# Kernel tuning notes

Hardware: AMD Instinct MI355X
Metric: run time of the kernel (lower is better)

## Reference

```python
import jax, jax.numpy as jnp
import numpy as np

B, N, D, H, WIN = 8, 4096, 768, 8, 8
HD = D // H
FG = N // 2 + 1
FL = WIN // 2 + 1


def _gelu(x):
    return jax.nn.gelu(x, approximate=False)


def _cgelu(z):
    # magnitude-based complex GELU: z * gelu(|z|) / (|z| + 1e-6)
    mag = jnp.abs(z)
    return z * (_gelu(mag) / (mag + 1e-6))


def setup_inputs():
    key = jax.random.key(0)
    ks = jax.random.split(key, 8)

    def w(k, shape):
        return jax.random.normal(k, shape, dtype=jnp.float32) * 0.02

    return {
        "x": jax.random.normal(ks[0], (B, N, D), dtype=jnp.float32),
        "ln_w": jnp.ones((D,), jnp.float32),
        "ln_b": jnp.zeros((D,), jnp.float32),
        "bf_g": jnp.ones((H, FG, 1), jnp.float32),
        "bb_g": jnp.full((H, FG, 1), -0.1, jnp.float32),
        "bf_l": jnp.ones((H, FL, 1), jnp.float32),
        "bb_l": jnp.full((H, FL, 1), -0.1, jnp.float32),
        "w1g": w(ks[1], (D, D)),
        "b1g": jnp.zeros((D,), jnp.float32),
        "w2g": w(ks[2], (D, H * FG * 2)),
        "b2g": jnp.zeros((H * FG * 2,), jnp.float32),
        "w1l": w(ks[3], (D, D)),
        "b1l": jnp.zeros((D,), jnp.float32),
        "w2l": w(ks[4], (D, H * FL * 2)),
        "b2l": jnp.zeros((H * FL * 2,), jnp.float32),
        "wf1": w(ks[5], (D, D // 2)),
        "bf1": jnp.zeros((D // 2,), jnp.float32),
        "wf2": w(ks[6], (D // 2, H)),
        "bf2": jnp.zeros((H,), jnp.float32),
    }


def reference(x, ln_w, ln_b, bf_g, bb_g, bf_l, bb_l, w1g, b1g, w2g, b2g,
              w1l, b1l, w2l, b2l, wf1, bf1, wf2, bf2):
    # pre-norm (LayerNorm, eps=1e-5)
    mu = jnp.mean(x, axis=-1, keepdims=True)
    var = jnp.mean((x - mu) ** 2, axis=-1, keepdims=True)
    xn = (x - mu) / jnp.sqrt(var + 1e-5) * ln_w + ln_b
    xh = xn.reshape(B, N, H, HD).transpose(0, 2, 1, 3)  # (B,H,N,HD)
    ctx = xn.mean(axis=1)  # (B,D)

    # ---- global branch: Hann-windowed rFFT over full sequence ----
    ag = (_gelu(ctx @ w1g + b1g) @ w2g + b2g).reshape(B, H, FG, 2)
    hann_g = jnp.hanning(N).astype(x.dtype)[None, None, :, None]
    Ff = jnp.fft.rfft(xh * hann_g, axis=2, norm="ortho")  # (B,H,FG,HD) complex
    eff_f = bf_g[None] * (1.0 + ag[..., 0:1])
    eff_b = bb_g[None] + ag[..., 1:2]
    x_global = jnp.fft.irfft(_cgelu(Ff * eff_f + eff_b), n=N, axis=2, norm="ortho")

    al = (_gelu(ctx @ w1l + b1l) @ w2l + b2l).reshape(B, H, FL, 2)
    nw = N // WIN
    hann_l = jnp.hanning(WIN).astype(x.dtype)[None, None, None, :, None]
    xw = xh.reshape(B, H, nw, WIN, HD) * hann_l
    Fl_fft = jnp.fft.rfft(xw, axis=3, norm="ortho")  # (B,H,nw,FL,HD)
    eff_fl = bf_l[None, :, None] * (1.0 + al[:, :, None, :, 0:1])
    eff_bl = bb_l[None, :, None] + al[:, :, None, :, 1:2]
    x_local = jnp.fft.irfft(_cgelu(Fl_fft * eff_fl + eff_bl), n=WIN, axis=3,
                            norm="ortho").reshape(B, H, N, HD)

    # ---- fusion gate ----
    alpha = jax.nn.sigmoid(_gelu(ctx @ wf1 + bf1) @ wf2 + bf2).reshape(B, H, 1, 1)
    fused = alpha * x_global + (1.0 - alpha) * x_local
    return x + fused.transpose(0, 2, 1, 3).reshape(B, N, D)
```

## Files before the change

kernel.cpp:

```cpp
#include <hip/hip_runtime.h>
#include <math.h>

#define B_ 8
#define N_ 4096
#define D_ 768
#define H_ 8
#define HD_ 96
#define FG_ 2049
#define TWO_PI 6.283185307179586476925f
#define PAD(i) ((i) + ((i) >> 5))

__device__ __forceinline__ float gelu_f(float x) {
    return 0.5f * x * (1.0f + erff(x * 0.7071067811865475f));
}

__global__ void k_zero(float* p, int n) {
    int i = blockIdx.x * 256 + threadIdx.x;
    if (i < n) p[i] = 0.f;
}

__global__ void k_layernorm(const float* __restrict__ x, const float* __restrict__ lw,
                            const float* __restrict__ lb, float* __restrict__ xn) {
    int row = blockIdx.x;
    const float* xr = x + (size_t)row * D_;
    float* xo = xn + (size_t)row * D_;
    int t = threadIdx.x;
    float v0 = xr[t], v1 = xr[t + 256], v2 = xr[t + 512];
    __shared__ float red[256];
    red[t] = v0 + v1 + v2;
    __syncthreads();
    for (int o = 128; o > 0; o >>= 1) { if (t < o) red[t] += red[t + o]; __syncthreads(); }
    float mu = red[0] * (1.0f / 768.0f);
    __syncthreads();
    float d0 = v0 - mu, d1 = v1 - mu, d2 = v2 - mu;
    red[t] = d0 * d0 + d1 * d1 + d2 * d2;
    __syncthreads();
    for (int o = 128; o > 0; o >>= 1) { if (t < o) red[t] += red[t + o]; __syncthreads(); }
    float rstd = rsqrtf(red[0] * (1.0f / 768.0f) + 1e-5f);
    xo[t]       = d0 * rstd * lw[t]       + lb[t];
    xo[t + 256] = d1 * rstd * lw[t + 256] + lb[t + 256];
    xo[t + 512] = d2 * rstd * lw[t + 512] + lb[t + 512];
}

__global__ void k_ctx(const float* __restrict__ xn, float* __restrict__ ctx) {
    int bx = blockIdx.x;
    int dchunk = bx % 3, nchunk = (bx / 3) % 16, b = bx / 48;
    int d = dchunk * 256 + threadIdx.x;
    const float* base = xn + (size_t)b * N_ * D_ + d;
    int n0 = nchunk * 256;
    float s = 0.f;
    for (int i = 0; i < 256; ++i) s += base[(size_t)(n0 + i) * D_];
    atomicAdd(ctx + b * D_ + d, s * (1.0f / 4096.0f));
}

__global__ void k_transpose(const float* __restrict__ src, float* __restrict__ dst) {
    __shared__ float tile[64][65];
    int d0 = blockIdx.x * 64, n0 = blockIdx.y * 64, b = blockIdx.z;
    int c = threadIdx.x & 63, r4 = threadIdx.x >> 6;
    for (int q = 0; q < 16; ++q) {
        int r = r4 * 16 + q;
        tile[r][c] = src[((size_t)b * N_ + n0 + r) * D_ + d0 + c];
    }
    __syncthreads();
    for (int q = 0; q < 16; ++q) {
        int r = r4 * 16 + q;
        dst[((size_t)b * D_ + d0 + r) * N_ + n0 + c] = tile[c][r];
    }
}

__global__ void k_mlp1(const float* __restrict__ ctx,
                       const float* __restrict__ w1g, const float* __restrict__ b1g,
                       const float* __restrict__ w1l, const float* __restrict__ b1l,
                       const float* __restrict__ wf1, const float* __restrict__ bf1,
                       float* __restrict__ h1g, float* __restrict__ h1l, float* __restrict__ hf) {
    __shared__ float cl[B_ * D_];
    for (int i = threadIdx.x; i < B_ * D_; i += 256) cl[i] = ctx[i];
    __syncthreads();
    int c = blockIdx.x * 256 + threadIdx.x;
    if (c >= 1920) return;
    const float *w, *bias; float* out; int ncol, cc;
    if (c < 768)      { w = w1g; bias = b1g; out = h1g; ncol = 768; cc = c; }
    else if (c < 1536){ w = w1l; bias = b1l; out = h1l; ncol = 768; cc = c - 768; }
    else              { w = wf1; bias = bf1; out = hf;  ncol = 384; cc = c - 1536; }
    float acc[B_];
    #pragma unroll
    for (int b = 0; b < B_; ++b) acc[b] = 0.f;
    for (int d = 0; d < 768; ++d) {
        float wv = w[(size_t)d * ncol + cc];
        #pragma unroll
        for (int b = 0; b < B_; ++b) acc[b] += cl[b * 768 + d] * wv;
    }
    float bv = bias[cc];
    for (int b = 0; b < B_; ++b) out[b * ncol + cc] = gelu_f(acc[b] + bv);
}

__global__ void k_biasinit(const float* __restrict__ b2g, const float* __restrict__ b2l,
                           float* __restrict__ ag, float* __restrict__ al) {
    int c = blockIdx.x * 256 + threadIdx.x;
    const int CG = H_ * FG_ * 2;
    if (c < CG) {
        float v = b2g[c];
        for (int b = 0; b < B_; ++b) ag[(size_t)b * CG + c] = v;
    } else if (c < CG + 80) {
        int cc = c - CG;
        float v = b2l[cc];
        for (int b = 0; b < B_; ++b) al[b * 80 + cc] = v;
    }
}

__global__ void k_mlp2(const float* __restrict__ h1g, const float* __restrict__ h1l,
                       const float* __restrict__ hf,
                       const float* __restrict__ w2g, const float* __restrict__ w2l,
                       const float* __restrict__ wf2, const float* __restrict__ bf2,
                       float* __restrict__ ag, float* __restrict__ al, float* __restrict__ gate) {
    int kc = blockIdx.y;
    int d0 = kc * 192;
    __shared__ float lg[B_ * 192];
    __shared__ float ll[B_ * 192];
    for (int i = threadIdx.x; i < B_ * 192; i += 256) {
        int bb = i / 192, dd = i % 192;
        lg[i] = h1g[bb * 768 + d0 + dd];
        ll[i] = h1l[bb * 768 + d0 + dd];
    }
    __syncthreads();
    int c = blockIdx.x * 256 + threadIdx.x;
    const int CG = H_ * FG_ * 2;
    float acc[B_];
    #pragma unroll
    for (int b = 0; b < B_; ++b) acc[b] = 0.f;
    if (c < CG) {
        for (int d = 0; d < 192; ++d) {
            float wv = w2g[(size_t)(d0 + d) * CG + c];
            #pragma unroll
            for (int b = 0; b < B_; ++b) acc[b] += lg[b * 192 + d] * wv;
        }
        for (int b = 0; b < B_; ++b) atomicAdd(ag + (size_t)b * CG + c, acc[b]);
    } else if (c < CG + 80) {
        int cc = c - CG;
        for (int d = 0; d < 192; ++d) {
            float wv = w2l[(d0 + d) * 80 + cc];
            #pragma unroll
            for (int b = 0; b < B_; ++b) acc[b] += ll[b * 192 + d] * wv;
        }
        for (int b = 0; b < B_; ++b) atomicAdd(al + b * 80 + cc, acc[b]);
    } else if (c < CG + 88 && kc == 0) {
        int cc = c - CG - 80;
        for (int d = 0; d < 384; ++d) {
            float wv = wf2[d * 8 + cc];
            #pragma unroll
            for (int b = 0; b < B_; ++b) acc[b] += hf[b * 384 + d] * wv;
        }
        for (int b = 0; b < B_; ++b)
            gate[b * 8 + cc] = 1.0f / (1.0f + expf(-(acc[b] + bf2[cc])));
    }
}

__device__ __forceinline__ void fft_stages(float* re, float* im,
                                           const float* twr, const float* twi,
                                           int t, float sign) {
    for (int s = 1; s <= 12; ++s) {
        int half = 1 << (s - 1);
        int sh = 12 - s;
        for (int j = t; j < 2048; j += 256) {
            int grp = j >> (s - 1);
            int pos = j & (half - 1);
            int i1 = (grp << s) + pos;
            int i2 = i1 + half;
            int pt = PAD(pos << sh);
            int p1 = PAD(i1), p2 = PAD(i2);
            float wr = twr[pt], wi = sign * twi[pt];
            float ar = re[p1], ai = im[p1];
            float br = re[p2], bi = im[p2];
            float tr = br * wr - bi * wi;
            float tii = br * wi + bi * wr;
            re[p1] = ar + tr;  im[p1] = ai + tii;
            re[p2] = ar - tr;  im[p2] = ai - tii;
        }
        __syncthreads();
    }
}

__global__ __launch_bounds__(256) void k_spectral(
        const float* __restrict__ xt,
        const float* __restrict__ ag,
        const float* __restrict__ al,
        const float* __restrict__ gate,
        const float* __restrict__ bf_g, const float* __restrict__ bb_g,
        const float* __restrict__ bf_l, const float* __restrict__ bb_l,
        float* __restrict__ fused)
{
    __shared__ float re[4224];
    __shared__ float im[4224];
    __shared__ float twr[2112];
    __shared__ float twi[2112];
    int line0 = blockIdx.x * 2;
    int d0 = line0 % 768, b = line0 / 768;
    int h = d0 / HD_;
    int t = threadIdx.x;

    for (int k = t; k < 2048; k += 256) {
        float s, c;
        sincosf(-TWO_PI * (float)k / 4096.0f, &s, &c);
        twr[PAD(k)] = c; twi[PAD(k)] = s;
    }

    const float* src0 = xt + (size_t)line0 * N_;
    const float* src1 = src0 + N_;
    float raw0[16], raw1[16];
    #pragma unroll
    for (int q = 0; q < 4; ++q) {
        float4 v0 = ((const float4*)src0)[t * 4 + q];
        float4 v1 = ((const float4*)src1)[t * 4 + q];
        raw0[q * 4 + 0] = v0.x; raw0[q * 4 + 1] = v0.y;
        raw0[q * 4 + 2] = v0.z; raw0[q * 4 + 3] = v0.w;
        raw1[q * 4 + 0] = v1.x; raw1[q * 4 + 1] = v1.y;
        raw1[q * 4 + 2] = v1.z; raw1[q * 4 + 3] = v1.w;
    }
    #pragma unroll
    for (int i = 0; i < 16; ++i) {
        int n = t * 16 + i;
        float wn = 0.5f - 0.5f * cosf(TWO_PI * (float)n / 4095.0f);
        int r = PAD((int)(__brev((unsigned)n) >> 20));
        re[r] = raw0[i] * wn;
        im[r] = raw1[i] * wn;
    }

    float alc = gate[b * 8 + h];
    const float* alb = al + b * 80;
    float effl_f[5], effl_b[5];
    #pragma unroll
    for (int f = 0; f < 5; ++f) {
        int idx = h * 5 + f;
        effl_f[f] = bf_l[idx] * (1.0f + alb[idx * 2]);
        effl_b[f] = bb_l[idx] + alb[idx * 2 + 1];
    }
    const float s8 = 0.3535533905932738f;
    const float c7 = 0.7071067811865476f;
    const float cosT[8] = {1.f, c7, 0.f, -c7, -1.f, -c7, 0.f, c7};
    const float sinT[8] = {0.f, c7, 1.f, c7, 0.f, -c7, -1.f, -c7};
    float hl[8];
    #pragma unroll
    for (int j = 0; j < 8; ++j) hl[j] = 0.5f - 0.5f * cosf(TWO_PI * (float)j / 7.0f);
    float xl0[16], xl1[16];
    #pragma unroll
    for (int ln = 0; ln < 2; ++ln) {
        float* rawp = ln ? raw1 : raw0;
        float* xlp  = ln ? xl1 : xl0;
        #pragma unroll
        for (int w2 = 0; w2 < 2; ++w2) {
            float xw[8];
            #pragma unroll
            for (int j = 0; j < 8; ++j) xw[j] = rawp[w2 * 8 + j] * hl[j];
            float Yr[5], Yi[5];
            #pragma unroll
            for (int f = 0; f < 5; ++f) {
                float fr = 0.f, fi = 0.f;
                #pragma unroll
                for (int j = 0; j < 8; ++j) {
                    int k8 = (f * j) & 7;
                    fr += xw[j] * cosT[k8];
                    fi -= xw[j] * sinT[k8];
                }
                fr *= s8; fi *= s8;
                float zr = fr * effl_f[f] + effl_b[f];
                float zi = fi * effl_f[f];
                float mag = sqrtf(zr * zr + zi * zi);
                float g = gelu_f(mag) / (mag + 1e-6f);
                Yr[f] = zr * g; Yi[f] = zi * g;
            }
            #pragma unroll
            for (int j = 0; j < 8; ++j) {
                float acc = Yr[0] + Yr[4] * ((j & 1) ? -1.f : 1.f);
                #pragma unroll
                for (int f = 1; f < 4; ++f) {
                    int k8 = (f * j) & 7;
                    acc += 2.f * (Yr[f] * cosT[k8] - Yi[f] * sinT[k8]);
                }
                xlp[w2 * 8 + j] = acc * s8;
            }
        }
    }

    __syncthreads();
    fft_stages(re, im, twr, twi, t, 1.0f);

    const float inv64 = 1.0f / 64.0f;
    const float* agb = ag + (size_t)b * 32784;
    for (int k = t; k < 2048; k += 256) {
        int km = (4096 - k) & 4095;
        int pk = PAD(k), pm = PAD(km);
        float Zr = re[pk], Zi = im[pk];
        float Zr2 = re[pm], Zi2 = im[pm];
        float X0r = 0.5f * (Zr + Zr2), X0i = 0.5f * (Zi - Zi2);
        float X1r = 0.5f * (Zi + Zi2), X1i = -0.5f * (Zr - Zr2);
        int idx = h * FG_ + k;
        float efff = bf_g[idx] * (1.0f + agb[idx * 2]);
        float effb = bb_g[idx] + agb[idx * 2 + 1];
        float z0r = X0r * inv64 * efff + effb, z0i = X0i * inv64 * efff;
        float m0 = sqrtf(z0r * z0r + z0i * z0i);
        float g0 = gelu_f(m0) / (m0 + 1e-6f);
        float Y0r = z0r * g0, Y0i = z0i * g0;
        float z1r = X1r * inv64 * efff + effb, z1i = X1i * inv64 * efff;
        float m1 = sqrtf(z1r * z1r + z1i * z1i);
        float g1 = gelu_f(m1) / (m1 + 1e-6f);
        float Y1r = z1r * g1, Y1i = z1i * g1;
        re[pk] = Y0r - Y1i;  im[pk] = Y0i + Y1r;
        if (k) { re[pm] = Y0r + Y1i; im[pm] = Y1r - Y0i; }
    }
    if (t == 0) {
        int pk = PAD(2048);
        float Zr = re[pk], Zi = im[pk];
        int idx = h * FG_ + 2048;
        float efff = bf_g[idx] * (1.0f + agb[idx * 2]);
        float effb = bb_g[idx] + agb[idx * 2 + 1];
        float z0r = Zr * inv64 * efff + effb;
        float m0 = fabsf(z0r);
        float Y0r = z0r * (gelu_f(m0) / (m0 + 1e-6f));
        float z1r = Zi * inv64 * efff + effb;
        float m1 = fabsf(z1r);
        float Y1r = z1r * (gelu_f(m1) / (m1 + 1e-6f));
        re[pk] = Y0r;  im[pk] = Y1r;
    }
    __syncthreads();
    for (int n = t; n < 4096; n += 256) {
        int r = (int)(__brev((unsigned)n) >> 20);
        if (r > n) {
            int pn = PAD(n), pr = PAD(r);
            float a = re[pn]; re[pn] = re[pr]; re[pr] = a;
            float bb2 = im[pn]; im[pn] = im[pr]; im[pr] = bb2;
        }
    }
    __syncthreads();
    fft_stages(re, im, twr, twi, t, -1.0f);

    float* dst0 = fused + (size_t)line0 * N_;
    float* dst1 = dst0 + N_;
    float one_m = 1.0f - alc;
    #pragma unroll
    for (int q = 0; q < 4; ++q) {
        float4 v0, v1;
        int base = t * 16 + q * 4;
        v0.x = alc * re[PAD(base + 0)] * inv64 + one_m * xl0[q * 4 + 0];
        v0.y = alc * re[PAD(base + 1)] * inv64 + one_m * xl0[q * 4 + 1];
        v0.z = alc * re[PAD(base + 2)] * inv64 + one_m * xl0[q * 4 + 2];
        v0.w = alc * re[PAD(base + 3)] * inv64 + one_m * xl0[q * 4 + 3];
        v1.x = alc * im[PAD(base + 0)] * inv64 + one_m * xl1[q * 4 + 0];
        v1.y = alc * im[PAD(base + 1)] * inv64 + one_m * xl1[q * 4 + 1];
        v1.z = alc * im[PAD(base + 2)] * inv64 + one_m * xl1[q * 4 + 2];
        v1.w = alc * im[PAD(base + 3)] * inv64 + one_m * xl1[q * 4 + 3];
        ((float4*)dst0)[t * 4 + q] = v0;
        ((float4*)dst1)[t * 4 + q] = v1;
    }
}

__global__ void k_addout(const float* __restrict__ fused, const float* __restrict__ x,
                         float* __restrict__ out) {
    __shared__ float tile[64][65];
    int d0 = blockIdx.x * 64, n0 = blockIdx.y * 64, b = blockIdx.z;
    int c = threadIdx.x & 63, r4 = threadIdx.x >> 6;
    for (int q = 0; q < 16; ++q) {
        int r = r4 * 16 + q;
        tile[r][c] = fused[((size_t)b * D_ + d0 + r) * N_ + n0 + c];
    }
    __syncthreads();
    for (int q = 0; q < 16; ++q) {
        int r = r4 * 16 + q;
        size_t o = ((size_t)b * N_ + n0 + r) * D_ + d0 + c;
        out[o] = x[o] + tile[c][r];
    }
}

extern "C" void kernel_launch(void* const* d_in, const int* in_sizes, int n_in,
                              void* d_out, int out_size, void* d_ws, size_t ws_size,
                              hipStream_t stream) {
    const float* x    = (const float*)d_in[0];
    const float* ln_w = (const float*)d_in[1];
    const float* ln_b = (const float*)d_in[2];
    const float* bf_g = (const float*)d_in[3];
    const float* bb_g = (const float*)d_in[4];
    const float* bf_l = (const float*)d_in[5];
    const float* bb_l = (const float*)d_in[6];
    const float* w1g  = (const float*)d_in[7];
    const float* b1g  = (const float*)d_in[8];
    const float* w2g  = (const float*)d_in[9];
    const float* b2g  = (const float*)d_in[10];
    const float* w1l  = (const float*)d_in[11];
    const float* b1l  = (const float*)d_in[12];
    const float* w2l  = (const float*)d_in[13];
    const float* b2l  = (const float*)d_in[14];
    const float* wf1  = (const float*)d_in[15];
    const float* bf1  = (const float*)d_in[16];
    const float* wf2  = (const float*)d_in[17];
    const float* bf2  = (const float*)d_in[18];
    float* out = (float*)d_out;

    char* ws = (char*)d_ws;
    const size_t big = (size_t)B_ * D_ * N_ * sizeof(float);
    float* XT  = (float*)ws; ws += big;
    float* XN  = (float*)ws; ws += big;
    float* ctx = (float*)ws; ws += (size_t)B_ * D_ * 4;
    float* h1g = (float*)ws; ws += (size_t)B_ * 768 * 4;
    float* h1l = (float*)ws; ws += (size_t)B_ * 768 * 4;
    float* hf  = (float*)ws; ws += (size_t)B_ * 384 * 4;
    float* ag  = (float*)ws; ws += (size_t)B_ * 32784 * 4;
    float* alb = (float*)ws; ws += (size_t)B_ * 80 * 4;
    float* gat = (float*)ws; ws += (size_t)B_ * 8 * 4;

    k_zero<<<24, 256, 0, stream>>>(ctx, B_ * D_);
    k_layernorm<<<B_ * N_, 256, 0, stream>>>(x, ln_w, ln_b, XN);
    k_ctx<<<384, 256, 0, stream>>>(XN, ctx);
    k_transpose<<<dim3(12, 64, 8), 256, 0, stream>>>(XN, XT);
    k_mlp1<<<8, 256, 0, stream>>>(ctx, w1g, b1g, w1l, b1l, wf1, bf1, h1g, h1l, hf);
    k_biasinit<<<129, 256, 0, stream>>>(b2g, b2l, ag, alb);
    k_mlp2<<<dim3(129, 4), 256, 0, stream>>>(h1g, h1l, hf, w2g, w2l, wf2, bf2, ag, alb, gat);
    k_spectral<<<B_ * D_ / 2, 256, 0, stream>>>(XT, ag, alb, gat, bf_g, bb_g, bf_l, bb_l, XN);
    k_addout<<<dim3(12, 64, 8), 256, 0, stream>>>(XN, x, out);
}
```

Baseline: 706.7 us.

## Fuse layernorm into transpose, precompute twiddles, register-resident FFT stages

```diff
diff --git a/kernel.cpp b/kernel.cpp
--- a/kernel.cpp
+++ b/kernel.cpp
@@ -19,52 +19,72 @@
     if (i < n) p[i] = 0.f;
 }
 
-__global__ void k_layernorm(const float* __restrict__ x, const float* __restrict__ lw,
-                            const float* __restrict__ lb, float* __restrict__ xn) {
-    int row = blockIdx.x;
-    const float* xr = x + (size_t)row * D_;
-    float* xo = xn + (size_t)row * D_;
-    int t = threadIdx.x;
-    float v0 = xr[t], v1 = xr[t + 256], v2 = xr[t + 512];
-    __shared__ float red[256];
-    red[t] = v0 + v1 + v2;
-    __syncthreads();
-    for (int o = 128; o > 0; o >>= 1) { if (t < o) red[t] += red[t + o]; __syncthreads(); }
-    float mu = red[0] * (1.0f / 768.0f);
-    __syncthreads();
-    float d0 = v0 - mu, d1 = v1 - mu, d2 = v2 - mu;
-    red[t] = d0 * d0 + d1 * d1 + d2 * d2;
-    __syncthreads();
-    for (int o = 128; o > 0; o >>= 1) { if (t < o) red[t] += red[t + o]; __syncthreads(); }
-    float rstd = rsqrtf(red[0] * (1.0f / 768.0f) + 1e-5f);
-    xo[t]       = d0 * rstd * lw[t]       + lb[t];
-    xo[t + 256] = d1 * rstd * lw[t + 256] + lb[t + 256];
-    xo[t + 512] = d2 * rstd * lw[t + 512] + lb[t + 512];
-}
-
-__global__ void k_ctx(const float* __restrict__ xn, float* __restrict__ ctx) {
-    int bx = blockIdx.x;
-    int dchunk = bx % 3, nchunk = (bx / 3) % 16, b = bx / 48;
-    int d = dchunk * 256 + threadIdx.x;
-    const float* base = xn + (size_t)b * N_ * D_ + d;
-    int n0 = nchunk * 256;
-    float s = 0.f;
-    for (int i = 0; i < 256; ++i) s += base[(size_t)(n0 + i) * D_];
-    atomicAdd(ctx + b * D_ + d, s * (1.0f / 4096.0f));
-}
-
-__global__ void k_transpose(const float* __restrict__ src, float* __restrict__ dst) {
+__global__ void k_tables(float2* __restrict__ twg, float* __restrict__ hanng) {
+    int i = blockIdx.x * 256 + threadIdx.x;
+    if (i < 2048) {
+        float s, c;
+        sincosf(-TWO_PI * (float)i / 4096.0f, &s, &c);
+        twg[i] = make_float2(c, s);
+    }
+    if (i < 4096) hanng[i] = 0.5f - 0.5f * cosf(TWO_PI * (float)i / 4095.0f);
+}
+
+__global__ __launch_bounds__(256) void k_stats(const float* __restrict__ x,
+                                               float* __restrict__ mu,
+                                               float* __restrict__ rstd) {
+    int row = blockIdx.x * 4 + (threadIdx.x >> 6);
+    int lane = threadIdx.x & 63;
+    const float4* xr = (const float4*)(x + (size_t)row * D_);
+    float4 a = xr[lane], b = xr[lane + 64], c = xr[lane + 128];
+    float s = a.x + a.y + a.z + a.w + b.x + b.y + b.z + b.w + c.x + c.y + c.z + c.w;
+    #pragma unroll
+    for (int o = 32; o > 0; o >>= 1) s += __shfl_xor(s, o);
+    float m = s * (1.0f / 768.0f);
+    float v = 0.f, d;
+    d = a.x - m; v += d * d; d = a.y - m; v += d * d;
+    d = a.z - m; v += d * d; d = a.w - m; v += d * d;
+    d = b.x - m; v += d * d; d = b.y - m; v += d * d;
+    d = b.z - m; v += d * d; d = b.w - m; v += d * d;
+    d = c.x - m; v += d * d; d = c.y - m; v += d * d;
+    d = c.z - m; v += d * d; d = c.w - m; v += d * d;
+    #pragma unroll
+    for (int o = 32; o > 0; o >>= 1) v += __shfl_xor(v, o);
+    if (lane == 0) {
+        mu[row] = m;
+        rstd[row] = rsqrtf(v * (1.0f / 768.0f) + 1e-5f);
+    }
+}
+
+__global__ __launch_bounds__(256) void k_lnT(const float* __restrict__ x,
+                                             const float* __restrict__ mu,
+                                             const float* __restrict__ rstd,
+                                             const float* __restrict__ lw,
+                                             const float* __restrict__ lb,
+                                             float* __restrict__ xt,
+                                             float* __restrict__ ctx) {
     __shared__ float tile[64][65];
+    __shared__ float csum[4][64];
     int d0 = blockIdx.x * 64, n0 = blockIdx.y * 64, b = blockIdx.z;
     int c = threadIdx.x & 63, r4 = threadIdx.x >> 6;
+    float w = lw[d0 + c], bias = lb[d0 + c];
+    float partial = 0.f;
+    #pragma unroll
     for (int q = 0; q < 16; ++q) {
         int r = r4 * 16 + q;
-        tile[r][c] = src[((size_t)b * N_ + n0 + r) * D_ + d0 + c];
-    }
-    __syncthreads();
+        int row = b * N_ + n0 + r;
+        float v = (x[(size_t)row * D_ + d0 + c] - mu[row]) * rstd[row] * w + bias;
+        tile[r][c] = v;
+        partial += v;
+    }
+    csum[r4][c] = partial;
+    __syncthreads();
+    if (r4 == 0)
+        atomicAdd(ctx + b * D_ + d0 + c,
+                  (csum[0][c] + csum[1][c] + csum[2][c] + csum[3][c]) * (1.0f / 4096.0f));
+    #pragma unroll
     for (int q = 0; q < 16; ++q) {
         int r = r4 * 16 + q;
-        dst[((size_t)b * D_ + d0 + r) * N_ + n0 + c] = tile[c][r];
+        xt[((size_t)b * D_ + d0 + r) * N_ + n0 + c] = tile[c][r];
     }
 }
 
@@ -114,11 +134,11 @@
                        const float* __restrict__ wf2, const float* __restrict__ bf2,
                        float* __restrict__ ag, float* __restrict__ al, float* __restrict__ gate) {
     int kc = blockIdx.y;
-    int d0 = kc * 192;
-    __shared__ float lg[B_ * 192];
-    __shared__ float ll[B_ * 192];
-    for (int i = threadIdx.x; i < B_ * 192; i += 256) {
-        int bb = i / 192, dd = i % 192;
+    int d0 = kc * 96;
+    __shared__ float lg[B_ * 96];
+    __shared__ float ll[B_ * 96];
+    for (int i = threadIdx.x; i < B_ * 96; i += 256) {
+        int bb = i / 96, dd = i % 96;
         lg[i] = h1g[bb * 768 + d0 + dd];
         ll[i] = h1l[bb * 768 + d0 + dd];
     }
@@ -129,18 +149,18 @@
     #pragma unroll
     for (int b = 0; b < B_; ++b) acc[b] = 0.f;
     if (c < CG) {
-        for (int d = 0; d < 192; ++d) {
+        for (int d = 0; d < 96; ++d) {
             float wv = w2g[(size_t)(d0 + d) * CG + c];
             #pragma unroll
-            for (int b = 0; b < B_; ++b) acc[b] += lg[b * 192 + d] * wv;
+            for (int b = 0; b < B_; ++b) acc[b] += lg[b * 96 + d] * wv;
         }
         for (int b = 0; b < B_; ++b) atomicAdd(ag + (size_t)b * CG + c, acc[b]);
     } else if (c < CG + 80) {
         int cc = c - CG;
-        for (int d = 0; d < 192; ++d) {
+        for (int d = 0; d < 96; ++d) {
             float wv = w2l[(d0 + d) * 80 + cc];
             #pragma unroll
-            for (int b = 0; b < B_; ++b) acc[b] += ll[b * 192 + d] * wv;
+            for (int b = 0; b < B_; ++b) acc[b] += ll[b * 96 + d] * wv;
         }
         for (int b = 0; b < B_; ++b) atomicAdd(al + b * 80 + cc, acc[b]);
     } else if (c < CG + 88 && kc == 0) {
@@ -155,54 +175,95 @@
     }
 }
 
-__device__ __forceinline__ void fft_stages(float* re, float* im,
-                                           const float* twr, const float* twi,
-                                           int t, float sign) {
-    for (int s = 1; s <= 12; ++s) {
+__device__ __forceinline__ void fft_pass(float2* z, const float2* tw4,
+                                         const float2* __restrict__ twg,
+                                         int t, float sign) {
+    float2 v[16];
+    #pragma unroll
+    for (int i = 0; i < 16; ++i) v[i] = z[PAD(t * 16 + i)];
+    const float TC[8] = {1.f, 0.92387953251f, 0.70710678119f, 0.38268343236f,
+                         0.f, -0.38268343236f, -0.70710678119f, -0.92387953251f};
+    const float TS[8] = {0.f, -0.38268343236f, -0.70710678119f, -0.92387953251f,
+                         -1.f, -0.92387953251f, -0.70710678119f, -0.38268343236f};
+    #pragma unroll
+    for (int s = 1; s <= 4; ++s) {
+        int half = 1 << (s - 1);
+        #pragma unroll
+        for (int u = 0; u < 8; ++u) {
+            int lg = u >> (s - 1), pos = u & (half - 1);
+            int i1 = (lg << s) + pos, i2 = i1 + half;
+            int m = pos << (4 - s);
+            float wr = TC[m], wi = sign * TS[m];
+            float2 a = v[i1], bb = v[i2];
+            float tr = bb.x * wr - bb.y * wi;
+            float ti = bb.x * wi + bb.y * wr;
+            v[i1] = make_float2(a.x + tr, a.y + ti);
+            v[i2] = make_float2(a.x - tr, a.y - ti);
+        }
+    }
+    #pragma unroll
+    for (int i = 0; i < 16; ++i) z[PAD(t * 16 + i)] = v[i];
+    __syncthreads();
+    for (int s = 5; s <= 10; ++s) {
         int half = 1 << (s - 1);
         int sh = 12 - s;
-        for (int j = t; j < 2048; j += 256) {
+        #pragma unroll
+        for (int u = 0; u < 8; ++u) {
+            int j = t + (u << 8);
             int grp = j >> (s - 1);
             int pos = j & (half - 1);
             int i1 = (grp << s) + pos;
-            int i2 = i1 + half;
-            int pt = PAD(pos << sh);
-            int p1 = PAD(i1), p2 = PAD(i2);
-            float wr = twr[pt], wi = sign * twi[pt];
-            float ar = re[p1], ai = im[p1];
-            float br = re[p2], bi = im[p2];
-            float tr = br * wr - bi * wi;
-            float tii = br * wi + bi * wr;
-            re[p1] = ar + tr;  im[p1] = ai + tii;
-            re[p2] = ar - tr;  im[p2] = ai - tii;
+            int p1 = PAD(i1), p2 = PAD(i1 + half);
+            float2 w = tw4[PAD(pos << (sh - 2))];
+            float wi = sign * w.y;
+            float2 a = z[p1], bb = z[p2];
+            float tr = bb.x * w.x - bb.y * wi;
+            float ti = bb.x * wi + bb.y * w.x;
+            z[p1] = make_float2(a.x + tr, a.y + ti);
+            z[p2] = make_float2(a.x - tr, a.y - ti);
         }
         __syncthreads();
     }
-}
-
-__global__ __launch_bounds__(256) void k_spectral(
+    for (int s = 11; s <= 12; ++s) {
+        int half = 1 << (s - 1);
+        int sh = 12 - s;
+        #pragma unroll
+        for (int u = 0; u < 8; ++u) {
+            int j = t + (u << 8);
+            int grp = j >> (s - 1);
+            int pos = j & (half - 1);
+            int i1 = (grp << s) + pos;
+            int p1 = PAD(i1), p2 = PAD(i1 + half);
+            float2 w = twg[pos << sh];
+            float wi = sign * w.y;
+            float2 a = z[p1], bb = z[p2];
+            float tr = bb.x * w.x - bb.y * wi;
+            float ti = bb.x * wi + bb.y * w.x;
+            z[p1] = make_float2(a.x + tr, a.y + ti);
+            z[p2] = make_float2(a.x - tr, a.y - ti);
+        }
+        __syncthreads();
+    }
+}
+
+__global__ __launch_bounds__(256, 4) void k_spectral(
         const float* __restrict__ xt,
         const float* __restrict__ ag,
         const float* __restrict__ al,
         const float* __restrict__ gate,
         const float* __restrict__ bf_g, const float* __restrict__ bb_g,
         const float* __restrict__ bf_l, const float* __restrict__ bb_l,
+        const float2* __restrict__ twg, const float* __restrict__ hanng,
         float* __restrict__ fused)
 {
-    __shared__ float re[4224];
-    __shared__ float im[4224];
-    __shared__ float twr[2112];
-    __shared__ float twi[2112];
+    __shared__ float2 z[4224];
+    __shared__ float2 tw4[528];
     int line0 = blockIdx.x * 2;
     int d0 = line0 % 768, b = line0 / 768;
     int h = d0 / HD_;
     int t = threadIdx.x;
 
-    for (int k = t; k < 2048; k += 256) {
-        float s, c;
-        sincosf(-TWO_PI * (float)k / 4096.0f, &s, &c);
-        twr[PAD(k)] = c; twi[PAD(k)] = s;
-    }
+    for (int m = t; m < 512; m += 256) tw4[PAD(m)] = twg[4 * m];
 
     const float* src0 = xt + (size_t)line0 * N_;
     const float* src1 = src0 + N_;
@@ -217,12 +278,17 @@
         raw1[q * 4 + 2] = v1.z; raw1[q * 4 + 3] = v1.w;
     }
     #pragma unroll
-    for (int i = 0; i < 16; ++i) {
-        int n = t * 16 + i;
-        float wn = 0.5f - 0.5f * cosf(TWO_PI * (float)n / 4095.0f);
-        int r = PAD((int)(__brev((unsigned)n) >> 20));
-        re[r] = raw0[i] * wn;
-        im[r] = raw1[i] * wn;
+    for (int q = 0; q < 4; ++q) {
+        float4 hw = ((const float4*)hanng)[t * 4 + q];
+        int nb = t * 16 + q * 4;
+        int r0 = PAD((int)(__brev((unsigned)(nb + 0)) >> 20));
+        int r1 = PAD((int)(__brev((unsigned)(nb + 1)) >> 20));
+        int r2 = PAD((int)(__brev((unsigned)(nb + 2)) >> 20));
+        int r3 = PAD((int)(__brev((unsigned)(nb + 3)) >> 20));
+        z[r0] = make_float2(raw0[q * 4 + 0] * hw.x, raw1[q * 4 + 0] * hw.x);
+        z[r1] = make_float2(raw0[q * 4 + 1] * hw.y, raw1[q * 4 + 1] * hw.y);
+        z[r2] = make_float2(raw0[q * 4 + 2] * hw.z, raw1[q * 4 + 2] * hw.z);
+        z[r3] = make_float2(raw0[q * 4 + 3] * hw.w, raw1[q * 4 + 3] * hw.w);
     }
 
     float alc = gate[b * 8 + h];
@@ -238,9 +304,8 @@
     const float c7 = 0.7071067811865476f;
     const float cosT[8] = {1.f, c7, 0.f, -c7, -1.f, -c7, 0.f, c7};
     const float sinT[8] = {0.f, c7, 1.f, c7, 0.f, -c7, -1.f, -c7};
-    float hl[8];
-    #pragma unroll
-    for (int j = 0; j < 8; ++j) hl[j] = 0.5f - 0.5f * cosf(TWO_PI * (float)j / 7.0f);
+    const float hl[8] = {0.f, 0.18825510f, 0.61126047f, 0.95048444f,
+                         0.95048444f, 0.61126047f, 0.18825510f, 0.f};
     float xl0[16], xl1[16];
     #pragma unroll
     for (int ln = 0; ln < 2; ++ln) {
@@ -282,17 +347,16 @@
     }
 
     __syncthreads();
-    fft_stages(re, im, twr, twi, t, 1.0f);
+    fft_pass(z, tw4, twg, t, 1.0f);
 
     const float inv64 = 1.0f / 64.0f;
     const float* agb = ag + (size_t)b * 32784;
     for (int k = t; k < 2048; k += 256) {
         int km = (4096 - k) & 4095;
         int pk = PAD(k), pm = PAD(km);
-        float Zr = re[pk], Zi = im[pk];
-        float Zr2 = re[pm], Zi2 = im[pm];
-        float X0r = 0.5f * (Zr + Zr2), X0i = 0.5f * (Zi - Zi2);
-        float X1r = 0.5f * (Zi + Zi2), X1i = -0.5f * (Zr - Zr2);
+        float2 Z = z[pk], Z2 = z[pm];
+        float X0r = 0.5f * (Z.x + Z2.x), X0i = 0.5f * (Z.y - Z2.y);
+        float X1r = 0.5f * (Z.y + Z2.y), X1i = -0.5f * (Z.x - Z2.x);
         int idx = h * FG_ + k;
         float efff = bf_g[idx] * (1.0f + agb[idx * 2]);
         float effb = bb_g[idx] + agb[idx * 2 + 1];
@@ -304,50 +368,50 @@
         float m1 = sqrtf(z1r * z1r + z1i * z1i);
         float g1 = gelu_f(m1) / (m1 + 1e-6f);
         float Y1r = z1r * g1, Y1i = z1i * g1;
-        re[pk] = Y0r - Y1i;  im[pk] = Y0i + Y1r;
-        if (k) { re[pm] = Y0r + Y1i; im[pm] = Y1r - Y0i; }
+        z[pk] = make_float2(Y0r - Y1i, Y0i + Y1r);
+        if (k) z[pm] = make_float2(Y0r + Y1i, Y1r - Y0i);
     }
     if (t == 0) {
         int pk = PAD(2048);
-        float Zr = re[pk], Zi = im[pk];
+        float2 Z = z[pk];
         int idx = h * FG_ + 2048;
         float efff = bf_g[idx] * (1.0f + agb[idx * 2]);
         float effb = bb_g[idx] + agb[idx * 2 + 1];
-        float z0r = Zr * inv64 * efff + effb;
+        float z0r = Z.x * inv64 * efff + effb;
         float m0 = fabsf(z0r);
         float Y0r = z0r * (gelu_f(m0) / (m0 + 1e-6f));
-        float z1r = Zi * inv64 * efff + effb;
+        float z1r = Z.y * inv64 * efff + effb;
         float m1 = fabsf(z1r);
         float Y1r = z1r * (gelu_f(m1) / (m1 + 1e-6f));
-        re[pk] = Y0r;  im[pk] = Y1r;
+        z[pk] = make_float2(Y0r, Y1r);
     }
     __syncthreads();
     for (int n = t; n < 4096; n += 256) {
         int r = (int)(__brev((unsigned)n) >> 20);
         if (r > n) {
             int pn = PAD(n), pr = PAD(r);
-            float a = re[pn]; re[pn] = re[pr]; re[pr] = a;
-            float bb2 = im[pn]; im[pn] = im[pr]; im[pr] = bb2;
-        }
-    }
-    __syncthreads();
-    fft_stages(re, im, twr, twi, t, -1.0f);
+            float2 a = z[pn]; z[pn] = z[pr]; z[pr] = a;
+        }
+    }
+    __syncthreads();
+    fft_pass(z, tw4, twg, t, -1.0f);
 
     float* dst0 = fused + (size_t)line0 * N_;
     float* dst1 = dst0 + N_;
     float one_m = 1.0f - alc;
     #pragma unroll
     for (int q = 0; q < 4; ++q) {
-        float4 v0, v1;
         int base = t * 16 + q * 4;
-        v0.x = alc * re[PAD(base + 0)] * inv64 + one_m * xl0[q * 4 + 0];
-        v0.y = alc * re[PAD(base + 1)] * inv64 + one_m * xl0[q * 4 + 1];
-        v0.z = alc * re[PAD(base + 2)] * inv64 + one_m * xl0[q * 4 + 2];
-        v0.w = alc * re[PAD(base + 3)] * inv64 + one_m * xl0[q * 4 + 3];
-        v1.x = alc * im[PAD(base + 0)] * inv64 + one_m * xl1[q * 4 + 0];
-        v1.y = alc * im[PAD(base + 1)] * inv64 + one_m * xl1[q * 4 + 1];
-        v1.z = alc * im[PAD(base + 2)] * inv64 + one_m * xl1[q * 4 + 2];
-        v1.w = alc * im[PAD(base + 3)] * inv64 + one_m * xl1[q * 4 + 3];
+        float2 za = z[PAD(base + 0)], zb = z[PAD(base + 1)];
+        float2 zc = z[PAD(base + 2)], zd = z[PAD(base + 3)];
+        float4 v0 = make_float4(alc * za.x * inv64 + one_m * xl0[q * 4 + 0],
+                                alc * zb.x * inv64 + one_m * xl0[q * 4 + 1],
+                                alc * zc.x * inv64 + one_m * xl0[q * 4 + 2],
+                                alc * zd.x * inv64 + one_m * xl0[q * 4 + 3]);
+        float4 v1 = make_float4(alc * za.y * inv64 + one_m * xl1[q * 4 + 0],
+                                alc * zb.y * inv64 + one_m * xl1[q * 4 + 1],
+                                alc * zc.y * inv64 + one_m * xl1[q * 4 + 2],
+                                alc * zd.y * inv64 + one_m * xl1[q * 4 + 3]);
         ((float4*)dst0)[t * 4 + q] = v0;
         ((float4*)dst1)[t * 4 + q] = v1;
     }
@@ -397,7 +461,7 @@
     char* ws = (char*)d_ws;
     const size_t big = (size_t)B_ * D_ * N_ * sizeof(float);
     float* XT  = (float*)ws; ws += big;
-    float* XN  = (float*)ws; ws += big;
+    float* FU  = (float*)ws; ws += big;
     float* ctx = (float*)ws; ws += (size_t)B_ * D_ * 4;
     float* h1g = (float*)ws; ws += (size_t)B_ * 768 * 4;
     float* h1l = (float*)ws; ws += (size_t)B_ * 768 * 4;
@@ -405,14 +469,19 @@
     float* ag  = (float*)ws; ws += (size_t)B_ * 32784 * 4;
     float* alb = (float*)ws; ws += (size_t)B_ * 80 * 4;
     float* gat = (float*)ws; ws += (size_t)B_ * 8 * 4;
+    float2* twg = (float2*)ws; ws += 2048 * sizeof(float2);
+    float* hanng = (float*)ws; ws += 4096 * sizeof(float);
+    float* mu   = FU;
+    float* rstd = FU + 32768;
 
     k_zero<<<24, 256, 0, stream>>>(ctx, B_ * D_);
-    k_layernorm<<<B_ * N_, 256, 0, stream>>>(x, ln_w, ln_b, XN);
-    k_ctx<<<384, 256, 0, stream>>>(XN, ctx);
-    k_transpose<<<dim3(12, 64, 8), 256, 0, stream>>>(XN, XT);
+    k_tables<<<16, 256, 0, stream>>>(twg, hanng);
+    k_stats<<<8192, 256, 0, stream>>>(x, mu, rstd);
+    k_lnT<<<dim3(12, 64, 8), 256, 0, stream>>>(x, mu, rstd, ln_w, ln_b, XT, ctx);
     k_mlp1<<<8, 256, 0, stream>>>(ctx, w1g, b1g, w1l, b1l, wf1, bf1, h1g, h1l, hf);
     k_biasinit<<<129, 256, 0, stream>>>(b2g, b2l, ag, alb);
-    k_mlp2<<<dim3(129, 4), 256, 0, stream>>>(h1g, h1l, hf, w2g, w2l, wf2, bf2, ag, alb, gat);
-    k_spectral<<<B_ * D_ / 2, 256, 0, stream>>>(XT, ag, alb, gat, bf_g, bb_g, bf_l, bb_l, XN);
-    k_addout<<<dim3(12, 64, 8), 256, 0, stream>>>(XN, x, out);
-}
+    k_mlp2<<<dim3(129, 8), 256, 0, stream>>>(h1g, h1l, hf, w2g, w2l, wf2, bf2, ag, alb, gat);
+    k_spectral<<<B_ * D_ / 2, 256, 0, stream>>>(XT, ag, alb, gat, bf_g, bb_g, bf_l, bb_l,
+                                                twg, hanng, FU);
+    k_addout<<<dim3(12, 64, 8), 256, 0, stream>>>(FU, x, out);
+}
```

Result: no change. 700.9 us (-0.8%).
